# Kernel optimization log

Measured on AMD Instinct MI355X. Metric: run time of the kernel, lower is better.

The kernel has to match this reference:

```python
import jax, jax.numpy as jnp
import numpy as np

T, B, L = 40, 64, 80
D_IN = 256
H = 4 * D_IN  # 1024
A = 18


def _lstm_scan(x, h0, c0, W_ih, W_hh, b_ih, b_hh):
    # x: [S,B,in] -> outputs [S,B,H]; PyTorch gate order i,f,g,o
    b = b_ih + b_hh
    def step(carry, xt):
        h, c = carry
        g = xt @ W_ih.T + h @ W_hh.T + b
        i, f, gg, o = jnp.split(g, 4, axis=-1)
        c = jax.nn.sigmoid(f) * c + jax.nn.sigmoid(i) * jnp.tanh(gg)
        h = jax.nn.sigmoid(o) * jnp.tanh(c)
        return (h, c), h
    (h, c), ys = jax.lax.scan(step, (h0, c0), x)
    return ys, h, c


def setup_inputs() -> dict:
    key = jax.random.key(0)
    ks = jax.random.split(key, 24)
    def rn(k, shape, scale=0.02):
        return jax.random.normal(k, shape, dtype=jnp.float32) * scale
    return {
        "state": rn(ks[0], (T, B, D_IN), 1.0),
        "demonstration": rn(ks[1], (T, B, L, D_IN), 1.0),
        "demonstration_length": jax.random.randint(ks[2], (T, B), 1, L + 1, dtype=jnp.int32),
        "h0": jnp.zeros((B, H), jnp.float32),
        "c0": jnp.zeros((B, H), jnp.float32),
        "enc_Wih": rn(ks[3], (4 * H, D_IN)),
        "enc_Whh": rn(ks[4], (4 * H, H)),
        "enc_bih": rn(ks[5], (4 * H,)),
        "enc_bhh": rn(ks[6], (4 * H,)),
        "attn_W": rn(ks[7], (1, 2 * H)),
        "attn_b": rn(ks[8], (1,)),
        "comb_W": rn(ks[9], (H, H + D_IN)),
        "comb_b": rn(ks[10], (H,)),
        "lstm_Wih": rn(ks[11], (4 * H, H)),
        "lstm_Whh": rn(ks[12], (4 * H, H)),
        "lstm_bih": rn(ks[13], (4 * H,)),
        "lstm_bhh": rn(ks[14], (4 * H,)),
        "mid_W": rn(ks[15], (H, H)),
        "mid_b": rn(ks[16], (H,)),
        "out_W": rn(ks[17], (A, H)),
        "out_b": rn(ks[18], (A,)),
    }


def reference(state, demonstration, demonstration_length, h0, c0,
              enc_Wih, enc_Whh, enc_bih, enc_bhh,
              attn_W, attn_b, comb_W, comb_b,
              lstm_Wih, lstm_Whh, lstm_bih, lstm_bhh,
              mid_W, mid_b, out_W, out_b):
    lengths = demonstration_length[0]              # [B], only t=0 lengths used (as in original)
    demo0 = demonstration[0]                       # [B,L,D_IN], only t=0 demo used
    z = jnp.zeros((B, H), demo0.dtype)
    enc, _, _ = _lstm_scan(demo0.transpose(1, 0, 2), z, z,
                           enc_Wih, enc_Whh, enc_bih, enc_bhh)  # [L,B,H]
    enc = enc.transpose(1, 0, 2)                   # [B,L,H]
    mask = jnp.arange(L)[None, :] < lengths[:, None]  # [B,L]
    # attn(cat(enc, h)) == enc @ Wd^T + h @ Wh^T + b (split of the concat linear)
    Wd, Wh = attn_W[:, :H], attn_W[:, H:]          # [1,H] each
    score_d = (enc @ Wd.T)[..., 0] + attn_b[0]     # [B,L], constant over t
    lstm_b = lstm_bih + lstm_bhh

    def step(carry, obs_t):
        h, c = carry
        scores = score_d + h @ Wh.T                # [B,L] ([B,1] broadcast)
        scores = jnp.where(mask, scores, -jnp.inf)
        w = jax.nn.softmax(scores, axis=-1)        # masked softmax over demo steps
        attn_applied = jnp.einsum('bl,blh->bh', w, enc)
        x = jax.nn.relu(jnp.concatenate([attn_applied, obs_t], axis=-1) @ comb_W.T + comb_b)
        g = x @ lstm_Wih.T + h @ lstm_Whh.T + lstm_b
        i, f, gg, o = jnp.split(g, 4, axis=-1)
        c = jax.nn.sigmoid(f) * c + jax.nn.sigmoid(i) * jnp.tanh(gg)
        h = jax.nn.sigmoid(o) * jnp.tanh(c)
        m = h @ mid_W.T + mid_b                    # no activation between middle and output (as in source)
        q_t = m @ out_W.T + out_b
        return (h, c), q_t

    (h, c), q = jax.lax.scan(step, (h0, c0), state)  # q: [T,B,A]
    return q, h, c
```

## Files before the change

kernel.cpp:

```cpp
#include <hip/hip_runtime.h>
#include <hip/hip_bf16.h>

#define TT 40
#define BB 64
#define LL 80
#define DD 256
#define HH 1024
#define G4H 4096
#define AA 18
#define KENC 1280
#define KLSTM 2048
#define KCOMB 1280
#define NB 256
#define NT 256
#define QSZ (TT*BB*AA)

typedef __bf16 bf16x8 __attribute__((ext_vector_type(8)));
typedef float  f32x4  __attribute__((ext_vector_type(4)));

#define OFF_WENC   ((size_t)0)
#define OFF_WLSTM  (OFF_WENC  + (size_t)G4H*KENC*2)
#define OFF_WCOMB  (OFF_WLSTM + (size_t)G4H*KLSTM*2)
#define OFF_WMID   (OFF_WCOMB + (size_t)HH*KCOMB*2)
#define OFF_BIASE  (OFF_WMID  + (size_t)HH*HH*2)
#define OFF_BIASL  (OFF_BIASE + (size_t)G4H*4)
#define OFF_DEMO   (OFF_BIASL + (size_t)G4H*4)
#define OFF_STATE  (OFF_DEMO  + (size_t)BB*LL*DD*2)
#define OFF_ENC    (OFF_STATE + (size_t)TT*BB*DD*2)
#define OFF_HDEC   (OFF_ENC   + (size_t)BB*LL*HH*2)
#define OFF_XALL   (OFF_HDEC  + (size_t)TT*BB*HH*2)
#define OFF_MF     (OFF_XALL  + (size_t)TT*BB*HH*2)
#define OFF_ATTNS  (OFF_MF    + (size_t)TT*BB*HH*2)
#define OFF_CF     (OFF_ATTNS + (size_t)BB*HH*2)
#define OFF_HROT   (OFF_CF    + (size_t)BB*HH*4)
#define NSLOT_E    81
#define NSLOT_D    41
#define OFF_BAR    (OFF_HROT  + (size_t)(NSLOT_E+NSLOT_D)*BB*HH*2)
#define FLAG_STRIDE 16
#define BAR_BYTES  (NB*FLAG_STRIDE*4)

__device__ __forceinline__ float sigm(float x){ return 1.f/(1.f+__expf(-x)); }

__device__ __forceinline__ float wred_sum(float v){
#pragma unroll
  for (int s=32; s>0; s>>=1) v += __shfl_xor(v, s, 64);
  return v;
}
__device__ __forceinline__ float wred_max(float v){
#pragma unroll
  for (int s=32; s>0; s>>=1) v = fmaxf(v, __shfl_xor(v, s, 64));
  return v;
}

__device__ __forceinline__ unsigned pack_bf16(float a, float b){
  unsigned short ua = __builtin_bit_cast(unsigned short, (__bf16)a);
  unsigned short ub = __builtin_bit_cast(unsigned short, (__bf16)b);
  return (unsigned)ua | ((unsigned)ub << 16);
}

__device__ __forceinline__ void st_u32_sc(unsigned* p, unsigned v){
  __hip_atomic_store(p, v, __ATOMIC_RELAXED, __HIP_MEMORY_SCOPE_AGENT);
}
__device__ __forceinline__ void st_b16_sc(__bf16* p, float v){
  unsigned short u = __builtin_bit_cast(unsigned short, (__bf16)v);
  asm volatile("global_store_short %0, %1, off sc0 sc1"
               :: "v"(p), "v"((unsigned)u) : "memory");
}

__device__ __forceinline__ void gload_lds16(const void* g, void* l){
  __builtin_amdgcn_global_load_lds(
      (const __attribute__((address_space(1))) unsigned*)g,
      (__attribute__((address_space(3))) unsigned*)l, 16, 0, 0);
}

__device__ __forceinline__ void gbar_arrive(unsigned* flags, unsigned target, int bk){
  __syncthreads();
  if (threadIdx.x == 0) {
    __builtin_amdgcn_fence(__ATOMIC_RELEASE, "agent");
    __hip_atomic_store(flags + (size_t)bk*FLAG_STRIDE, target,
                       __ATOMIC_RELAXED, __HIP_MEMORY_SCOPE_AGENT);
  }
}
__device__ __forceinline__ void gbar_wait(unsigned* flags, unsigned target){
  if (threadIdx.x < 64) {
    unsigned long long spins = 0;
    for (;;) {
      unsigned a0 = __hip_atomic_load(flags + (size_t)threadIdx.x*FLAG_STRIDE,       __ATOMIC_RELAXED, __HIP_MEMORY_SCOPE_AGENT);
      unsigned a1 = __hip_atomic_load(flags + (size_t)(64+threadIdx.x)*FLAG_STRIDE,  __ATOMIC_RELAXED, __HIP_MEMORY_SCOPE_AGENT);
      unsigned a2 = __hip_atomic_load(flags + (size_t)(128+threadIdx.x)*FLAG_STRIDE, __ATOMIC_RELAXED, __HIP_MEMORY_SCOPE_AGENT);
      unsigned a3 = __hip_atomic_load(flags + (size_t)(192+threadIdx.x)*FLAG_STRIDE, __ATOMIC_RELAXED, __HIP_MEMORY_SCOPE_AGENT);
      bool ok = (a0 >= target) && (a1 >= target) && (a2 >= target) && (a3 >= target);
      if (__all((int)ok)) break;
      if (++spins > (1ull<<20)) break;
      __builtin_amdgcn_s_sleep(1);
    }
  }
  __syncthreads();
  asm volatile("" ::: "memory");
}

__global__ void k_pack_enc(const float* __restrict__ wih, const float* __restrict__ whh,
                           const float* __restrict__ bih, const float* __restrict__ bhh,
                           __bf16* __restrict__ dst, float* __restrict__ bias){
  int p = blockIdx.x;
  int gate = p & 3, jj = (p >> 2) & 3, bq = p >> 4;
  int orig = gate*HH + bq*4 + jj;
  if (threadIdx.x == 0) bias[p] = bih[orig] + bhh[orig];
  const float* s0 = wih + (size_t)orig*DD;
  const float* s1 = whh + (size_t)orig*HH;
  __bf16* d = dst + (size_t)p*KENC;
  for (int k = threadIdx.x; k < KENC; k += blockDim.x)
    d[k] = (__bf16)(k < DD ? s0[k] : s1[k-DD]);
}
__global__ void k_pack_lstm(const float* __restrict__ wih, const float* __restrict__ whh,
                            const float* __restrict__ bih, const float* __restrict__ bhh,
                            __bf16* __restrict__ dst, float* __restrict__ bias){
  int p = blockIdx.x;
  int gate = p & 3, jj = (p >> 2) & 3, bq = p >> 4;
  int orig = gate*HH + bq*4 + jj;
  if (threadIdx.x == 0) bias[p] = bih[orig] + bhh[orig];
  const float* s0 = wih + (size_t)orig*HH;
  const float* s1 = whh + (size_t)orig*HH;
  __bf16* d = dst + (size_t)p*KLSTM;
  for (int k = threadIdx.x; k < KLSTM; k += blockDim.x)
    d[k] = (__bf16)(k < HH ? s0[k] : s1[k-HH]);
}
__global__ void k_conv(const float* __restrict__ src, __bf16* __restrict__ dst, int n){
  int i = blockIdx.x*blockDim.x + threadIdx.x;
  if (i < n) dst[i] = (__bf16)src[i];
}

__global__ __launch_bounds__(NT, 1)
void k_main(const int* __restrict__ demlen,
            const float* __restrict__ h0, const float* __restrict__ c0,
            const float* __restrict__ attn_w,
            const float* __restrict__ comb_b, const float* __restrict__ mid_b,
            const float* __restrict__ out_w, const float* __restrict__ out_b,
            float* __restrict__ out, char* __restrict__ ws){
  const int bk = blockIdx.x, tid = threadIdx.x;
  const int wv = tid >> 6, ln = tid & 63;
  const int l15 = ln & 15, lhi = ln >> 4;
  const int klane = lhi * 8;
  const int gtid = bk*NT + tid;

  __bf16* wEnc  = (__bf16*)(ws + OFF_WENC);
  __bf16* wLstm = (__bf16*)(ws + OFF_WLSTM);
  __bf16* wComb = (__bf16*)(ws + OFF_WCOMB);
  __bf16* wMid  = (__bf16*)(ws + OFF_WMID);
  const float* bE = (const float*)(ws + OFF_BIASE);
  const float* bL = (const float*)(ws + OFF_BIASL);
  __bf16* demoC = (__bf16*)(ws + OFF_DEMO);
  __bf16* stateB= (__bf16*)(ws + OFF_STATE);
  __bf16* encB  = (__bf16*)(ws + OFF_ENC);
  __bf16* hdec  = (__bf16*)(ws + OFF_HDEC);
  __bf16* xall  = (__bf16*)(ws + OFF_XALL);
  __bf16* mf    = (__bf16*)(ws + OFF_MF);
  __bf16* attnS = (__bf16*)(ws + OFF_ATTNS);
  float*  cf    = (float*)(ws + OFF_CF);
  __bf16* hrotE = (__bf16*)(ws + OFF_HROT);
  __bf16* hrotD = hrotE + (size_t)NSLOT_E*BB*HH;
  unsigned* flags = (unsigned*)(ws + OFF_BAR);

  __shared__ __align__(16) char lds_h[BB*HH*2];
  __shared__ float g_lds[BB*17];
  __shared__ float sc_sh[LL];
  __shared__ float w_sh[LL];

  unsigned bar = 0;
  const int m_ = tid >> 1, q2 = tid & 1;
  const int j0_ = bk*4 + 2*q2;
  const int ar = wv*16 + l15;

  for (int i = gtid; i < BB*HH/2; i += NB*NT) st_u32_sc((unsigned*)hrotE + i, 0u);
  if (tid < 128) { cf[m_*HH + j0_] = 0.f; cf[m_*HH + j0_ + 1] = 0.f; }
  ++bar; gbar_arrive(flags, bar, bk);

  for (int t = 0; t < LL; ++t) {
    bf16x8 dv[8], bw[8];
    const __bf16* arow = demoC + ((size_t)ar*LL + t)*DD;
    const __bf16* brow = wEnc + (size_t)(bk*16 + l15)*KENC;
#pragma unroll
    for (int u = 0; u < 8; ++u) dv[u] = *(const bf16x8*)(arow + u*32 + klane);
#pragma unroll
    for (int u = 0; u < 8; ++u) bw[u] = *(const bf16x8*)(brow + u*32 + klane);
    __builtin_amdgcn_sched_barrier(0);
    gbar_wait(flags, bar);

    {
      const char* hRg = (const char*)(hrotE + (size_t)t*BB*HH);
#pragma unroll
      for (int u = 0; u < 32; ++u) {
        int chunk = u*4 + wv;
        gload_lds16(hRg + chunk*1024 + ln*16, lds_h + chunk*1024);
      }
    }
    __builtin_amdgcn_sched_barrier(0);

    f32x4 acc = {0.f,0.f,0.f,0.f};
#pragma unroll
    for (int u = 0; u < 8; ++u)
      acc = __builtin_amdgcn_mfma_f32_16x16x32_bf16(dv[u], bw[u], acc, 0,0,0);
    __syncthreads();
#pragma unroll 8
    for (int kk = 0; kk < HH; kk += 32) {
      int k0 = kk + klane;
      int off = (ar*2048 + k0*2) ^ ((ar & 7) << 4);
      acc = __builtin_amdgcn_mfma_f32_16x16x32_bf16(*(const bf16x8*)(lds_h + off),
                                                    *(const bf16x8*)(brow + DD + k0), acc, 0,0,0);
    }
    {
      int r0 = wv*16 + lhi*4;
#pragma unroll
      for (int r = 0; r < 4; ++r) g_lds[(r0+r)*17 + l15] = acc[r];
    }
    __syncthreads();
    if (tid < 128) {
      char* hWg = (char*)(hrotE + (size_t)(t+1)*BB*HH);
      int gb = m_*17 + q2*8, cb = bk*16 + q2*8;
      float gi0 = g_lds[gb+0]+bE[cb+0], gf0 = g_lds[gb+1]+bE[cb+1];
      float gg0 = g_lds[gb+2]+bE[cb+2], go0 = g_lds[gb+3]+bE[cb+3];
      float gi1 = g_lds[gb+4]+bE[cb+4], gf1 = g_lds[gb+5]+bE[cb+5];
      float gg1 = g_lds[gb+6]+bE[cb+6], go1 = g_lds[gb+7]+bE[cb+7];
      float cA = cf[m_*HH + j0_], cB = cf[m_*HH + j0_ + 1];
      float cn0 = sigm(gf0)*cA + sigm(gi0)*tanhf(gg0);
      float cn1 = sigm(gf1)*cB + sigm(gi1)*tanhf(gg1);
      float hn0 = sigm(go0)*tanhf(cn0);
      float hn1 = sigm(go1)*tanhf(cn1);
      cf[m_*HH + j0_] = cn0; cf[m_*HH + j0_ + 1] = cn1;
      unsigned hp = pack_bf16(hn0, hn1);
      int byte = (m_*2048 + j0_*2) ^ ((m_ & 7) << 4);
      st_u32_sc((unsigned*)(hWg + byte), hp);
      st_u32_sc((unsigned*)(encB + ((size_t)m_*LL + t)*HH + j0_), hp);
    }
    ++bar; gbar_arrive(flags, bar, bk);
  }

  gbar_wait(flags, bar);
  {
    int b = bk >> 2, qq = bk & 3;
    for (int i = 0; i < 20; ++i) {
      int l = wv*20 + i;
      const __bf16* er = encB + ((size_t)b*LL + l)*HH + ln*16;
      bf16x8 e0 = *(const bf16x8*)(er);
      bf16x8 e1 = *(const bf16x8*)(er + 8);
      float part = 0.f;
#pragma unroll
      for (int j = 0; j < 8; ++j) {
        part += (float)e0[j] * attn_w[ln*16 + j];
        part += (float)e1[j] * attn_w[ln*16 + 8 + j];
      }
      part = wred_sum(part);
      if (ln == 0) sc_sh[l] = part;
    }
    __syncthreads();
    if (wv == 0) {
      int len = demlen[b];
      float s0 = (ln < len) ? sc_sh[ln] : -1e30f;
      float s1 = (ln < 16 && 64+ln < len) ? sc_sh[64+ln] : -1e30f;
      float mx = wred_max(fmaxf(s0, s1));
      float e0 = __expf(s0 - mx);
      float e1 = (ln < 16) ? __expf(s1 - mx) : 0.f;
      float inv = 1.f / wred_sum(e0 + e1);
      w_sh[ln] = e0 * inv;
      if (ln < 16) w_sh[64+ln] = e1 * inv;
    }
    __syncthreads();
    int col = qq*256 + tid;
    float a = 0.f;
    const __bf16* eb = encB + (size_t)b*LL*HH + col;
#pragma unroll 4
    for (int l = 0; l < LL; ++l) a += w_sh[l] * (float)eb[(size_t)l*HH];
    st_b16_sc(attnS + (size_t)b*HH + col, a);
    for (int i = gtid; i < BB*HH; i += NB*NT) {
      int row = i >> 10;
      int byte = (i*2) ^ ((row & 7) << 4);
      st_b16_sc((__bf16*)((char*)hrotD + byte), h0[i]);
    }
    if (tid < 128) {
      cf[m_*HH + j0_]     = c0[m_*HH + j0_];
      cf[m_*HH + j0_ + 1] = c0[m_*HH + j0_ + 1];
    }
  }
  ++bar; gbar_arrive(flags, bar, bk);

  gbar_wait(flags, bar);
  {
    int g = bk*4 + wv;
    for (int i = 0; i < 10; ++i) {
      int ti = i*1024 + g;
      int mt = ti >> 6, nt = ti & 63;
      f32x4 acc = {0.f,0.f,0.f,0.f};
      const __bf16* brow = wComb + (size_t)(nt*16 + l15)*KCOMB;
      int r = mt*16 + l15, bb = r & 63;
      const __bf16* aat = attnS + (size_t)bb*HH;
      const __bf16* ast = stateB + (size_t)r*DD;
#pragma unroll 8
      for (int kk = 0; kk < KCOMB; kk += 32) {
        int k0 = kk + klane;
        bf16x8 af = (k0 < HH) ? *(const bf16x8*)(aat + k0)
                              : *(const bf16x8*)(ast + (k0-HH));
        acc = __builtin_amdgcn_mfma_f32_16x16x32_bf16(af, *(const bf16x8*)(brow + k0), acc, 0,0,0);
      }
      int col = nt*16 + l15;
      float cb = comb_b[col];
      int r0 = mt*16 + lhi*4;
#pragma unroll
      for (int rr = 0; rr < 4; ++rr)
        st_b16_sc(xall + (size_t)(r0+rr)*HH + col, fmaxf(acc[rr]+cb, 0.f));
    }
  }
  ++bar; gbar_arrive(flags, bar, bk);
  gbar_wait(flags, bar);

  for (int t = 0; t < TT; ++t) {
    bf16x8 xv[32], bw[32];
    const __bf16* xrow = xall + ((size_t)t*BB + ar)*HH;
    const __bf16* brow = wLstm + (size_t)(bk*16 + l15)*KLSTM;
#pragma unroll
    for (int u = 0; u < 32; ++u) xv[u] = *(const bf16x8*)(xrow + u*32 + klane);
#pragma unroll
    for (int u = 0; u < 32; ++u) bw[u] = *(const bf16x8*)(brow + u*32 + klane);
    __builtin_amdgcn_sched_barrier(0);
    gbar_wait(flags, bar);

    {
      const char* hRg = (const char*)(hrotD + (size_t)t*BB*HH);
#pragma unroll
      for (int u = 0; u < 32; ++u) {
        int chunk = u*4 + wv;
        gload_lds16(hRg + chunk*1024 + ln*16, lds_h + chunk*1024);
      }
    }
    __builtin_amdgcn_sched_barrier(0);

    f32x4 acc = {0.f,0.f,0.f,0.f};
#pragma unroll
    for (int u = 0; u < 32; ++u)
      acc = __builtin_amdgcn_mfma_f32_16x16x32_bf16(xv[u], bw[u], acc, 0,0,0);
    __syncthreads();
#pragma unroll 8
    for (int kk = 0; kk < HH; kk += 32) {
      int k0 = kk + klane;
      int off = (ar*2048 + k0*2) ^ ((ar & 7) << 4);
      acc = __builtin_amdgcn_mfma_f32_16x16x32_bf16(*(const bf16x8*)(lds_h + off),
                                                    *(const bf16x8*)(brow + HH + k0), acc, 0,0,0);
    }
    {
      int r0 = wv*16 + lhi*4;
#pragma unroll
      for (int r = 0; r < 4; ++r) g_lds[(r0+r)*17 + l15] = acc[r];
    }
    __syncthreads();
    if (tid < 128) {
      char* hWg = (char*)(hrotD + (size_t)(t+1)*BB*HH);
      int gb = m_*17 + q2*8, cb = bk*16 + q2*8;
      float gi0 = g_lds[gb+0]+bL[cb+0], gf0 = g_lds[gb+1]+bL[cb+1];
      float gg0 = g_lds[gb+2]+bL[cb+2], go0 = g_lds[gb+3]+bL[cb+3];
      float gi1 = g_lds[gb+4]+bL[cb+4], gf1 = g_lds[gb+5]+bL[cb+5];
      float gg1 = g_lds[gb+6]+bL[cb+6], go1 = g_lds[gb+7]+bL[cb+7];
      float cA = cf[m_*HH + j0_], cB = cf[m_*HH + j0_ + 1];
      float cn0 = sigm(gf0)*cA + sigm(gi0)*tanhf(gg0);
      float cn1 = sigm(gf1)*cB + sigm(gi1)*tanhf(gg1);
      float hn0 = sigm(go0)*tanhf(cn0);
      float hn1 = sigm(go1)*tanhf(cn1);
      cf[m_*HH + j0_] = cn0; cf[m_*HH + j0_ + 1] = cn1;
      unsigned hp = pack_bf16(hn0, hn1);
      int byte = (m_*2048 + j0_*2) ^ ((m_ & 7) << 4);
      st_u32_sc((unsigned*)(hWg + byte), hp);
      st_u32_sc((unsigned*)(hdec + ((size_t)t*BB + m_)*HH + j0_), hp);
      if (t == TT-1) {
        out[QSZ + m_*HH + j0_]     = hn0;
        out[QSZ + m_*HH + j0_ + 1] = hn1;
      }
    }
    ++bar; gbar_arrive(flags, bar, bk);
  }

  if (tid < 128) {
    out[QSZ + BB*HH + m_*HH + j0_]     = cf[m_*HH + j0_];
    out[QSZ + BB*HH + m_*HH + j0_ + 1] = cf[m_*HH + j0_ + 1];
  }

  gbar_wait(flags, bar);
  {
    int g = bk*4 + wv;
    for (int i = 0; i < 10; ++i) {
      int ti = i*1024 + g;
      int mt = ti >> 6, nt = ti & 63;
      f32x4 acc = {0.f,0.f,0.f,0.f};
      const __bf16* brow = wMid + (size_t)(nt*16 + l15)*HH;
      const __bf16* arow2 = hdec + (size_t)(mt*16 + l15)*HH;
#pragma unroll 8
      for (int kk = 0; kk < HH; kk += 32) {
        int k0 = kk + klane;
        acc = __builtin_amdgcn_mfma_f32_16x16x32_bf16(*(const bf16x8*)(arow2 + k0),
                                                      *(const bf16x8*)(brow + k0), acc, 0,0,0);
      }
      int col = nt*16 + l15;
      float mb = mid_b[col];
      int r0 = mt*16 + lhi*4;
#pragma unroll
      for (int rr = 0; rr < 4; ++rr)
        st_b16_sc(mf + (size_t)(r0+rr)*HH + col, acc[rr]+mb);
    }
  }
  ++bar; gbar_arrive(flags, bar, bk);

  gbar_wait(flags, bar);
  {
    int g = bk*4 + wv;
    for (int i = 0; i < 3; ++i) {
      int row = i*1024 + g;
      if (row < TT*BB) {
        const __bf16* mr = mf + (size_t)row*HH;
        float mreg[16];
#pragma unroll
        for (int k = 0; k < 16; ++k) mreg[k] = (float)mr[ln + 64*k];
        for (int a = 0; a < AA; ++a) {
          float p = 0.f;
#pragma unroll
          for (int k = 0; k < 16; ++k) p += mreg[k] * out_w[(size_t)a*HH + ln + 64*k];
          p = wred_sum(p);
          if (ln == 0) out[(size_t)row*AA + a] = p + out_b[a];
        }
      }
    }
  }
}

extern "C" void kernel_launch(void* const* d_in, const int* in_sizes, int n_in,
                              void* d_out, int out_size, void* d_ws, size_t ws_size,
                              hipStream_t stream) {
  (void)in_sizes; (void)n_in; (void)out_size; (void)ws_size;
  const float* state    = (const float*)d_in[0];
  const float* demo     = (const float*)d_in[1];
  const int*   demlen   = (const int*)d_in[2];
  const float* h0       = (const float*)d_in[3];
  const float* c0       = (const float*)d_in[4];
  const float* enc_wih  = (const float*)d_in[5];
  const float* enc_whh  = (const float*)d_in[6];
  const float* enc_bih  = (const float*)d_in[7];
  const float* enc_bhh  = (const float*)d_in[8];
  const float* attn_w   = (const float*)d_in[9];
  const float* comb_w   = (const float*)d_in[11];
  const float* comb_b   = (const float*)d_in[12];
  const float* lstm_wih = (const float*)d_in[13];
  const float* lstm_whh = (const float*)d_in[14];
  const float* lstm_bih = (const float*)d_in[15];
  const float* lstm_bhh = (const float*)d_in[16];
  const float* mid_w    = (const float*)d_in[17];
  const float* mid_b    = (const float*)d_in[18];
  const float* out_w    = (const float*)d_in[19];
  const float* out_b    = (const float*)d_in[20];
  char* ws = (char*)d_ws;

  (void)hipMemsetAsync(ws + OFF_BAR, 0, BAR_BYTES, stream);
  k_pack_enc <<<G4H, 256, 0, stream>>>(enc_wih, enc_whh, enc_bih, enc_bhh,
                                       (__bf16*)(ws + OFF_WENC), (float*)(ws + OFF_BIASE));
  k_pack_lstm<<<G4H, 256, 0, stream>>>(lstm_wih, lstm_whh, lstm_bih, lstm_bhh,
                                       (__bf16*)(ws + OFF_WLSTM), (float*)(ws + OFF_BIASL));
  k_conv<<<(HH*KCOMB + 255)/256, 256, 0, stream>>>(comb_w, (__bf16*)(ws + OFF_WCOMB), HH*KCOMB);
  k_conv<<<(HH*HH   + 255)/256, 256, 0, stream>>>(mid_w,  (__bf16*)(ws + OFF_WMID),  HH*HH);
  k_conv<<<(BB*LL*DD + 255)/256, 256, 0, stream>>>(demo,  (__bf16*)(ws + OFF_DEMO),  BB*LL*DD);
  k_conv<<<(TT*BB*DD + 255)/256, 256, 0, stream>>>(state, (__bf16*)(ws + OFF_STATE), TT*BB*DD);
  k_main<<<NB, NT, 0, stream>>>(demlen, h0, c0, attn_w, comb_b, mid_b,
                                out_w, out_b, (float*)d_out, ws);
}
```

Measured before the change: 2.241 ms.

## Double block threads, split recurrent K across wave halves, drop LDS h staging

Doubles threads per block to 512 and splits each recurrent step's K dimension between two groups of four waves, reducing the two partial gate sums through a second LDS buffer. The previous h state is now read directly from global memory (L2) instead of being copied into a 128KB LDS tile, and the weight/input prefetch before the grid barrier is removed. The cell state moves from a global buffer into registers, and the post-loop GEMM phases are re-indexed for eight waves per block. The aim is to shorten the serial per-step latency by halving each wave's MFMA chain. The cost is lost early prefetch before the barrier, unswizzled global reads of h, and an extra LDS reduction per step.

Result: faster. 2.125 ms (-5.2%).

```diff
diff --git a/kernel.cpp b/kernel.cpp
--- a/kernel.cpp
+++ b/kernel.cpp
@@ -12,7 +12,7 @@
 #define KLSTM 2048
 #define KCOMB 1280
 #define NB 256
-#define NT 256
+#define NT 512
 #define QSZ (TT*BB*AA)
 
 typedef __bf16 bf16x8 __attribute__((ext_vector_type(8)));
@@ -31,8 +31,7 @@
 #define OFF_XALL   (OFF_HDEC  + (size_t)TT*BB*HH*2)
 #define OFF_MF     (OFF_XALL  + (size_t)TT*BB*HH*2)
 #define OFF_ATTNS  (OFF_MF    + (size_t)TT*BB*HH*2)
-#define OFF_CF     (OFF_ATTNS + (size_t)BB*HH*2)
-#define OFF_HROT   (OFF_CF    + (size_t)BB*HH*4)
+#define OFF_HROT   (OFF_ATTNS + (size_t)BB*HH*2)
 #define NSLOT_E    81
 #define NSLOT_D    41
 #define OFF_BAR    (OFF_HROT  + (size_t)(NSLOT_E+NSLOT_D)*BB*HH*2)
@@ -65,12 +64,6 @@
   unsigned short u = __builtin_bit_cast(unsigned short, (__bf16)v);
   asm volatile("global_store_short %0, %1, off sc0 sc1"
                :: "v"(p), "v"((unsigned)u) : "memory");
-}
-
-__device__ __forceinline__ void gload_lds16(const void* g, void* l){
-  __builtin_amdgcn_global_load_lds(
-      (const __attribute__((address_space(1))) unsigned*)g,
-      (__attribute__((address_space(3))) unsigned*)l, 16, 0, 0);
 }
 
 __device__ __forceinline__ void gbar_arrive(unsigned* flags, unsigned target, int bk){
@@ -156,80 +149,63 @@
   __bf16* xall  = (__bf16*)(ws + OFF_XALL);
   __bf16* mf    = (__bf16*)(ws + OFF_MF);
   __bf16* attnS = (__bf16*)(ws + OFF_ATTNS);
-  float*  cf    = (float*)(ws + OFF_CF);
   __bf16* hrotE = (__bf16*)(ws + OFF_HROT);
   __bf16* hrotD = hrotE + (size_t)NSLOT_E*BB*HH;
   unsigned* flags = (unsigned*)(ws + OFF_BAR);
 
-  __shared__ __align__(16) char lds_h[BB*HH*2];
-  __shared__ float g_lds[BB*17];
+  __shared__ float g_lds [BB*17];
+  __shared__ float g_lds2[BB*17];
   __shared__ float sc_sh[LL];
   __shared__ float w_sh[LL];
 
   unsigned bar = 0;
   const int m_ = tid >> 1, q2 = tid & 1;
   const int j0_ = bk*4 + 2*q2;
-  const int ar = wv*16 + l15;
+  const int mt = wv & 3;
+  const int am = mt*16 + l15;
+  const int khalf = wv >> 2;
+
+  float cfa = 0.f, cfb = 0.f;
 
   for (int i = gtid; i < BB*HH/2; i += NB*NT) st_u32_sc((unsigned*)hrotE + i, 0u);
-  if (tid < 128) { cf[m_*HH + j0_] = 0.f; cf[m_*HH + j0_ + 1] = 0.f; }
   ++bar; gbar_arrive(flags, bar, bk);
 
   for (int t = 0; t < LL; ++t) {
-    bf16x8 dv[8], bw[8];
-    const __bf16* arow = demoC + ((size_t)ar*LL + t)*DD;
+    gbar_wait(flags, bar);
+    const __bf16* hR = hrotE + (size_t)t*BB*HH;
     const __bf16* brow = wEnc + (size_t)(bk*16 + l15)*KENC;
-#pragma unroll
-    for (int u = 0; u < 8; ++u) dv[u] = *(const bf16x8*)(arow + u*32 + klane);
-#pragma unroll
-    for (int u = 0; u < 8; ++u) bw[u] = *(const bf16x8*)(brow + u*32 + klane);
-    __builtin_amdgcn_sched_barrier(0);
-    gbar_wait(flags, bar);
-
+    const int kbase = khalf * 640;
+
+    f32x4 acc = {0.f,0.f,0.f,0.f};
+#pragma unroll 8
+    for (int kk = 0; kk < 640; kk += 32) {
+      int k0 = kbase + kk + klane;
+      const __bf16* pa = (k0 < DD) ? demoC + ((size_t)am*LL + t)*DD + k0
+                                   : hR + (size_t)am*HH + (k0 - DD);
+      acc = __builtin_amdgcn_mfma_f32_16x16x32_bf16(*(const bf16x8*)pa,
+                                                    *(const bf16x8*)(brow + k0), acc, 0,0,0);
+    }
     {
-      const char* hRg = (const char*)(hrotE + (size_t)t*BB*HH);
-#pragma unroll
-      for (int u = 0; u < 32; ++u) {
-        int chunk = u*4 + wv;
-        gload_lds16(hRg + chunk*1024 + ln*16, lds_h + chunk*1024);
-      }
-    }
-    __builtin_amdgcn_sched_barrier(0);
-
-    f32x4 acc = {0.f,0.f,0.f,0.f};
-#pragma unroll
-    for (int u = 0; u < 8; ++u)
-      acc = __builtin_amdgcn_mfma_f32_16x16x32_bf16(dv[u], bw[u], acc, 0,0,0);
-    __syncthreads();
-#pragma unroll 8
-    for (int kk = 0; kk < HH; kk += 32) {
-      int k0 = kk + klane;
-      int off = (ar*2048 + k0*2) ^ ((ar & 7) << 4);
-      acc = __builtin_amdgcn_mfma_f32_16x16x32_bf16(*(const bf16x8*)(lds_h + off),
-                                                    *(const bf16x8*)(brow + DD + k0), acc, 0,0,0);
-    }
-    {
-      int r0 = wv*16 + lhi*4;
-#pragma unroll
-      for (int r = 0; r < 4; ++r) g_lds[(r0+r)*17 + l15] = acc[r];
+      float* gl = khalf ? g_lds2 : g_lds;
+      int r0 = mt*16 + lhi*4;
+#pragma unroll
+      for (int r = 0; r < 4; ++r) gl[(r0+r)*17 + l15] = acc[r];
     }
     __syncthreads();
     if (tid < 128) {
       char* hWg = (char*)(hrotE + (size_t)(t+1)*BB*HH);
       int gb = m_*17 + q2*8, cb = bk*16 + q2*8;
-      float gi0 = g_lds[gb+0]+bE[cb+0], gf0 = g_lds[gb+1]+bE[cb+1];
-      float gg0 = g_lds[gb+2]+bE[cb+2], go0 = g_lds[gb+3]+bE[cb+3];
-      float gi1 = g_lds[gb+4]+bE[cb+4], gf1 = g_lds[gb+5]+bE[cb+5];
-      float gg1 = g_lds[gb+6]+bE[cb+6], go1 = g_lds[gb+7]+bE[cb+7];
-      float cA = cf[m_*HH + j0_], cB = cf[m_*HH + j0_ + 1];
-      float cn0 = sigm(gf0)*cA + sigm(gi0)*tanhf(gg0);
-      float cn1 = sigm(gf1)*cB + sigm(gi1)*tanhf(gg1);
+      float gi0 = g_lds[gb+0]+g_lds2[gb+0]+bE[cb+0], gf0 = g_lds[gb+1]+g_lds2[gb+1]+bE[cb+1];
+      float gg0 = g_lds[gb+2]+g_lds2[gb+2]+bE[cb+2], go0 = g_lds[gb+3]+g_lds2[gb+3]+bE[cb+3];
+      float gi1 = g_lds[gb+4]+g_lds2[gb+4]+bE[cb+4], gf1 = g_lds[gb+5]+g_lds2[gb+5]+bE[cb+5];
+      float gg1 = g_lds[gb+6]+g_lds2[gb+6]+bE[cb+6], go1 = g_lds[gb+7]+g_lds2[gb+7]+bE[cb+7];
+      float cn0 = sigm(gf0)*cfa + sigm(gi0)*tanhf(gg0);
+      float cn1 = sigm(gf1)*cfb + sigm(gi1)*tanhf(gg1);
       float hn0 = sigm(go0)*tanhf(cn0);
       float hn1 = sigm(go1)*tanhf(cn1);
-      cf[m_*HH + j0_] = cn0; cf[m_*HH + j0_ + 1] = cn1;
+      cfa = cn0; cfb = cn1;
       unsigned hp = pack_bf16(hn0, hn1);
-      int byte = (m_*2048 + j0_*2) ^ ((m_ & 7) << 4);
-      st_u32_sc((unsigned*)(hWg + byte), hp);
+      st_u32_sc((unsigned*)(hWg + m_*2048 + j0_*2), hp);
       st_u32_sc((unsigned*)(encB + ((size_t)m_*LL + t)*HH + j0_), hp);
     }
     ++bar; gbar_arrive(flags, bar, bk);
@@ -238,8 +214,8 @@
   gbar_wait(flags, bar);
   {
     int b = bk >> 2, qq = bk & 3;
-    for (int i = 0; i < 20; ++i) {
-      int l = wv*20 + i;
+    for (int i = 0; i < 10; ++i) {
+      int l = wv*10 + i;
       const __bf16* er = encB + ((size_t)b*LL + l)*HH + ln*16;
       bf16x8 e0 = *(const bf16x8*)(er);
       bf16x8 e1 = *(const bf16x8*)(er + 8);
@@ -265,33 +241,34 @@
       if (ln < 16) w_sh[64+ln] = e1 * inv;
     }
     __syncthreads();
-    int col = qq*256 + tid;
-    float a = 0.f;
-    const __bf16* eb = encB + (size_t)b*LL*HH + col;
+    if (tid < 256) {
+      int col = qq*256 + tid;
+      float a = 0.f;
+      const __bf16* eb = encB + (size_t)b*LL*HH + col;
 #pragma unroll 4
-    for (int l = 0; l < LL; ++l) a += w_sh[l] * (float)eb[(size_t)l*HH];
-    st_b16_sc(attnS + (size_t)b*HH + col, a);
-    for (int i = gtid; i < BB*HH; i += NB*NT) {
-      int row = i >> 10;
-      int byte = (i*2) ^ ((row & 7) << 4);
-      st_b16_sc((__bf16*)((char*)hrotD + byte), h0[i]);
+      for (int l = 0; l < LL; ++l) a += w_sh[l] * (float)eb[(size_t)l*HH];
+      st_b16_sc(attnS + (size_t)b*HH + col, a);
+    }
+    for (int i = gtid; i < BB*HH/2; i += NB*NT) {
+      int i2 = i*2;
+      st_u32_sc((unsigned*)hrotD + i, pack_bf16(h0[i2], h0[i2+1]));
     }
     if (tid < 128) {
-      cf[m_*HH + j0_]     = c0[m_*HH + j0_];
-      cf[m_*HH + j0_ + 1] = c0[m_*HH + j0_ + 1];
+      cfa = c0[m_*HH + j0_];
+      cfb = c0[m_*HH + j0_ + 1];
     }
   }
   ++bar; gbar_arrive(flags, bar, bk);
 
   gbar_wait(flags, bar);
   {
-    int g = bk*4 + wv;
-    for (int i = 0; i < 10; ++i) {
-      int ti = i*1024 + g;
-      int mt = ti >> 6, nt = ti & 63;
+    int g = bk*8 + wv;
+    for (int i = 0; i < 5; ++i) {
+      int ti = i*2048 + g;
+      int mtt = ti >> 6, nt = ti & 63;
       f32x4 acc = {0.f,0.f,0.f,0.f};
       const __bf16* brow = wComb + (size_t)(nt*16 + l15)*KCOMB;
-      int r = mt*16 + l15, bb = r & 63;
+      int r = mtt*16 + l15, bb = r & 63;
       const __bf16* aat = attnS + (size_t)bb*HH;
       const __bf16* ast = stateB + (size_t)r*DD;
 #pragma unroll 8
@@ -303,70 +280,50 @@
       }
       int col = nt*16 + l15;
       float cb = comb_b[col];
-      int r0 = mt*16 + lhi*4;
+      int r0 = mtt*16 + lhi*4;
 #pragma unroll
       for (int rr = 0; rr < 4; ++rr)
         st_b16_sc(xall + (size_t)(r0+rr)*HH + col, fmaxf(acc[rr]+cb, 0.f));
     }
   }
   ++bar; gbar_arrive(flags, bar, bk);
-  gbar_wait(flags, bar);
 
   for (int t = 0; t < TT; ++t) {
-    bf16x8 xv[32], bw[32];
-    const __bf16* xrow = xall + ((size_t)t*BB + ar)*HH;
+    gbar_wait(flags, bar);
+    const __bf16* hR = hrotD + (size_t)t*BB*HH;
     const __bf16* brow = wLstm + (size_t)(bk*16 + l15)*KLSTM;
-#pragma unroll
-    for (int u = 0; u < 32; ++u) xv[u] = *(const bf16x8*)(xrow + u*32 + klane);
-#pragma unroll
-    for (int u = 0; u < 32; ++u) bw[u] = *(const bf16x8*)(brow + u*32 + klane);
-    __builtin_amdgcn_sched_barrier(0);
-    gbar_wait(flags, bar);
-
-    {
-      const char* hRg = (const char*)(hrotD + (size_t)t*BB*HH);
-#pragma unroll
-      for (int u = 0; u < 32; ++u) {
-        int chunk = u*4 + wv;
-        gload_lds16(hRg + chunk*1024 + ln*16, lds_h + chunk*1024);
-      }
-    }
-    __builtin_amdgcn_sched_barrier(0);
+    const int kbase = khalf * HH;
+    const __bf16* arow = khalf ? (hR + (size_t)am*HH)
+                               : (xall + ((size_t)t*BB + am)*HH);
 
     f32x4 acc = {0.f,0.f,0.f,0.f};
-#pragma unroll
-    for (int u = 0; u < 32; ++u)
-      acc = __builtin_amdgcn_mfma_f32_16x16x32_bf16(xv[u], bw[u], acc, 0,0,0);
-    __syncthreads();
 #pragma unroll 8
     for (int kk = 0; kk < HH; kk += 32) {
       int k0 = kk + klane;
-      int off = (ar*2048 + k0*2) ^ ((ar & 7) << 4);
-      acc = __builtin_amdgcn_mfma_f32_16x16x32_bf16(*(const bf16x8*)(lds_h + off),
-                                                    *(const bf16x8*)(brow + HH + k0), acc, 0,0,0);
+      acc = __builtin_amdgcn_mfma_f32_16x16x32_bf16(*(const bf16x8*)(arow + k0),
+                                                    *(const bf16x8*)(brow + kbase + k0), acc, 0,0,0);
     }
     {
-      int r0 = wv*16 + lhi*4;
-#pragma unroll
-      for (int r = 0; r < 4; ++r) g_lds[(r0+r)*17 + l15] = acc[r];
+      float* gl = khalf ? g_lds2 : g_lds;
+      int r0 = mt*16 + lhi*4;
+#pragma unroll
+      for (int r = 0; r < 4; ++r) gl[(r0+r)*17 + l15] = acc[r];
     }
     __syncthreads();
     if (tid < 128) {
       char* hWg = (char*)(hrotD + (size_t)(t+1)*BB*HH);
       int gb = m_*17 + q2*8, cb = bk*16 + q2*8;
-      float gi0 = g_lds[gb+0]+bL[cb+0], gf0 = g_lds[gb+1]+bL[cb+1];
-      float gg0 = g_lds[gb+2]+bL[cb+2], go0 = g_lds[gb+3]+bL[cb+3];
-      float gi1 = g_lds[gb+4]+bL[cb+4], gf1 = g_lds[gb+5]+bL[cb+5];
-      float gg1 = g_lds[gb+6]+bL[cb+6], go1 = g_lds[gb+7]+bL[cb+7];
-      float cA = cf[m_*HH + j0_], cB = cf[m_*HH + j0_ + 1];
-      float cn0 = sigm(gf0)*cA + sigm(gi0)*tanhf(gg0);
-      float cn1 = sigm(gf1)*cB + sigm(gi1)*tanhf(gg1);
+      float gi0 = g_lds[gb+0]+g_lds2[gb+0]+bL[cb+0], gf0 = g_lds[gb+1]+g_lds2[gb+1]+bL[cb+1];
+      float gg0 = g_lds[gb+2]+g_lds2[gb+2]+bL[cb+2], go0 = g_lds[gb+3]+g_lds2[gb+3]+bL[cb+3];
+      float gi1 = g_lds[gb+4]+g_lds2[gb+4]+bL[cb+4], gf1 = g_lds[gb+5]+g_lds2[gb+5]+bL[cb+5];
+      float gg1 = g_lds[gb+6]+g_lds2[gb+6]+bL[cb+6], go1 = g_lds[gb+7]+g_lds2[gb+7]+bL[cb+7];
+      float cn0 = sigm(gf0)*cfa + sigm(gi0)*tanhf(gg0);
+      float cn1 = sigm(gf1)*cfb + sigm(gi1)*tanhf(gg1);
       float hn0 = sigm(go0)*tanhf(cn0);
       float hn1 = sigm(go1)*tanhf(cn1);
-      cf[m_*HH + j0_] = cn0; cf[m_*HH + j0_ + 1] = cn1;
+      cfa = cn0; cfb = cn1;
       unsigned hp = pack_bf16(hn0, hn1);
-      int byte = (m_*2048 + j0_*2) ^ ((m_ & 7) << 4);
-      st_u32_sc((unsigned*)(hWg + byte), hp);
+      st_u32_sc((unsigned*)(hWg + m_*2048 + j0_*2), hp);
       st_u32_sc((unsigned*)(hdec + ((size_t)t*BB + m_)*HH + j0_), hp);
       if (t == TT-1) {
         out[QSZ + m_*HH + j0_]     = hn0;
@@ -377,19 +334,19 @@
   }
 
   if (tid < 128) {
-    out[QSZ + BB*HH + m_*HH + j0_]     = cf[m_*HH + j0_];
-    out[QSZ + BB*HH + m_*HH + j0_ + 1] = cf[m_*HH + j0_ + 1];
+    out[QSZ + BB*HH + m_*HH + j0_]     = cfa;
+    out[QSZ + BB*HH + m_*HH + j0_ + 1] = cfb;
   }
 
   gbar_wait(flags, bar);
   {
-    int g = bk*4 + wv;
-    for (int i = 0; i < 10; ++i) {
-      int ti = i*1024 + g;
-      int mt = ti >> 6, nt = ti & 63;
+    int g = bk*8 + wv;
+    for (int i = 0; i < 5; ++i) {
+      int ti = i*2048 + g;
+      int mtt = ti >> 6, nt = ti & 63;
       f32x4 acc = {0.f,0.f,0.f,0.f};
       const __bf16* brow = wMid + (size_t)(nt*16 + l15)*HH;
-      const __bf16* arow2 = hdec + (size_t)(mt*16 + l15)*HH;
+      const __bf16* arow2 = hdec + (size_t)(mtt*16 + l15)*HH;
 #pragma unroll 8
       for (int kk = 0; kk < HH; kk += 32) {
         int k0 = kk + klane;
@@ -398,7 +355,7 @@
       }
       int col = nt*16 + l15;
       float mb = mid_b[col];
-      int r0 = mt*16 + lhi*4;
+      int r0 = mtt*16 + lhi*4;
 #pragma unroll
       for (int rr = 0; rr < 4; ++rr)
         st_b16_sc(mf + (size_t)(r0+rr)*HH + col, acc[rr]+mb);
@@ -408,9 +365,9 @@
 
   gbar_wait(flags, bar);
   {
-    int g = bk*4 + wv;
-    for (int i = 0; i < 3; ++i) {
-      int row = i*1024 + g;
+    int g = bk*8 + wv;
+    for (int i = 0; i < 2; ++i) {
+      int row = i*2048 + g;
       if (row < TT*BB) {
         const __bf16* mr = mf + (size_t)row*HH;
         float mreg[16];
```
